# Performance work log

Measured on AMD Instinct MI355X. Metric: run time of the kernel, lower is better.

The kernel has to match this reference:

```python
import jax, jax.numpy as jnp
import numpy as np

NEG_SLOPE = 0.2  # PyG RGATConv default negative_slope


def _rgat_conv(x, src, dst, edge_type, W, q, k, b, num_nodes):
    # W: [R, in, H] per-relation weight (heads=1 so H = heads*out_channels)
    # Transform every node by every relation once, then gather per edge
    # (same math as PyG's per-edge bmm with index_select'd weights, but
    #  avoids materializing [E, in, H] weights).
    xr = jnp.einsum('ni,rio->rno', x, W)            # [R, N, H]
    qv = jnp.einsum('rno,oh->rnh', xr, q)           # [R, N, heads]
    kv = jnp.einsum('rno,oh->rnh', xr, k)           # [R, N, heads]
    # additive self-attention: alpha_e = leaky_relu(q(out_i) + k(out_j))
    alpha = qv[edge_type, dst] + kv[edge_type, src]  # [E, heads]
    alpha = jnp.where(alpha >= 0, alpha, NEG_SLOPE * alpha)
    # softmax over incoming edges of each destination node (across-relation)
    amax = jax.ops.segment_max(alpha, dst, num_segments=num_nodes)  # [N, heads]
    amax = jnp.where(jnp.isfinite(amax), amax, 0.0)
    ex = jnp.exp(alpha - amax[dst])
    denom = jax.ops.segment_sum(ex, dst, num_segments=num_nodes)
    att = ex / (denom[dst] + 1e-16)                 # [E, heads]
    msg = xr[edge_type, src] * att                  # [E, H] (heads=1 broadcast)
    out = jax.ops.segment_sum(msg, dst, num_segments=num_nodes)    # [N, H]
    return out + b


def setup_inputs() -> dict:
    key = jax.random.key(0)
    ks = jax.random.split(key, 16)
    N, E, R, IN, H = 50000, 800000, 8, 128, 128
    x = jax.random.normal(ks[0], (N, IN), dtype=jnp.float32)
    edge_index = jax.random.randint(ks[1], (2, E), 0, N, dtype=jnp.int32)
    edge_type = jax.random.randint(ks[2], (E,), 0, R, dtype=jnp.int32)
    s_in = 1.0 / np.sqrt(IN)
    s_h = 1.0 / np.sqrt(H)
    w0 = jax.random.normal(ks[3], (R, IN, H), dtype=jnp.float32) * s_in
    q0 = jax.random.normal(ks[4], (H, 1), dtype=jnp.float32) * s_h
    k0 = jax.random.normal(ks[5], (H, 1), dtype=jnp.float32) * s_h
    b0 = jnp.zeros((H,), dtype=jnp.float32)
    w1 = jax.random.normal(ks[6], (R, H, H), dtype=jnp.float32) * s_h
    q1 = jax.random.normal(ks[7], (H, 1), dtype=jnp.float32) * s_h
    k1 = jax.random.normal(ks[8], (H, 1), dtype=jnp.float32) * s_h
    b1 = jnp.zeros((H,), dtype=jnp.float32)
    fc1_w = jax.random.normal(ks[9], (2 * H, H), dtype=jnp.float32) * (1.0 / np.sqrt(2 * H))
    fc1_b = jnp.zeros((H,), dtype=jnp.float32)
    fc2_w = jax.random.normal(ks[10], (H, 1), dtype=jnp.float32) * s_h
    fc2_b = jnp.zeros((1,), dtype=jnp.float32)
    return {"x": x, "edge_index": edge_index, "edge_type": edge_type,
            "w0": w0, "q0": q0, "k0": k0, "b0": b0,
            "w1": w1, "q1": q1, "k1": k1, "b1": b1,
            "fc1_w": fc1_w, "fc1_b": fc1_b, "fc2_w": fc2_w, "fc2_b": fc2_b}


def reference(x, edge_index, edge_type, w0, q0, k0, b0, w1, q1, k1, b1, fc1_w, fc1_b, fc2_w, fc2_b):
    N = x.shape[0]
    src, dst = edge_index[0], edge_index[1]
    h = jax.nn.relu(_rgat_conv(x, src, dst, edge_type, w0, q0, k0, b0, N))
    h = jax.nn.relu(_rgat_conv(h, src, dst, edge_type, w1, q1, k1, b1, N))
    g = jnp.concatenate([h.mean(axis=0), h.max(axis=0)], axis=-1)  # [2H]
    g = jnp.tanh(g)
    g = jax.nn.relu(g @ fc1_w + fc1_b)   # dropout is identity in eval mode
    out = g @ fc2_w + fc2_b              # [1]
    return jax.nn.sigmoid(out)
```

## Files before the change

kernel.cpp:

```cpp
#include <hip/hip_runtime.h>
#include <hip/hip_bf16.h>


typedef __bf16 bf16x8 __attribute__((ext_vector_type(8)));
typedef __bf16 bf16x4 __attribute__((ext_vector_type(4)));
typedef __bf16 bf16x2 __attribute__((ext_vector_type(2)));
typedef float f32x4 __attribute__((ext_vector_type(4)));

#define CBSH 10
#define CSC_CH 4096


__global__ __launch_bounds__(256) void k_chist(const int* __restrict__ dst, int* __restrict__ chist, int E) {
  __shared__ int lh[64];
  int t = threadIdx.x;
  if (t < 64) lh[t] = 0;
  __syncthreads();
  for (int e = blockIdx.x * 256 + t; e < E; e += gridDim.x * 256)
    atomicAdd(&lh[dst[e] >> CBSH], 1);
  __syncthreads();
  if (t < 64 && lh[t]) atomicAdd(&chist[t], lh[t]);
}

__global__ void k_cscan(const int* __restrict__ chist, int* __restrict__ cbase, int* __restrict__ ccur,
                        int ncb, int E) {
  if (threadIdx.x == 0) {
    int acc = 0;
    for (int i = 0; i < ncb; ++i) { cbase[i] = acc; ccur[i] = acc; acc += chist[i]; }
    cbase[ncb] = E;
  }
}

__global__ __launch_bounds__(256) void k_cscatter(const int* __restrict__ src, const int* __restrict__ dst,
                                                  const int* __restrict__ et, int* __restrict__ ccur,
                                                  int* __restrict__ tmp, int E) {
  __shared__ int recbuf[CSC_CH];
  __shared__ int lcnt[64], lbase[64], gbase[64], lcur[64];
  int t = threadIdx.x;
  int base = blockIdx.x * CSC_CH;
  int cnt = E - base; if (cnt > CSC_CH) cnt = CSC_CH;
  if (t < 64) lcnt[t] = 0;
  __syncthreads();
  int myrec[CSC_CH / 256], mycb[CSC_CH / 256];
  int k = 0;
  for (int i = t; i < cnt; i += 256, ++k) {
    int d = dst[base + i];
    int cb = d >> CBSH;
    myrec[k] = src[base + i] | (et[base + i] << 17) | ((d & ((1 << CBSH) - 1)) << 20);
    mycb[k] = cb;
    atomicAdd(&lcnt[cb], 1);
  }
  __syncthreads();
  if (t == 0) {
    int acc = 0;
    for (int c = 0; c < 64; ++c) { lbase[c] = acc; lcur[c] = acc; acc += lcnt[c]; }
  }
  __syncthreads();
  if (t < 64 && lcnt[t] > 0) gbase[t] = atomicAdd(&ccur[t], lcnt[t]);
  __syncthreads();
  k = 0;
  for (int i = t; i < cnt; i += 256, ++k) {
    int p = atomicAdd(&lcur[mycb[k]], 1);
    recbuf[p] = myrec[k];
  }
  __syncthreads();
  for (int i = t; i < cnt; i += 256) {
    int lo = 0, hi = 63;
    while (lo < hi) { int mid = (lo + hi + 1) >> 1; if (lbase[mid] <= i) lo = mid; else hi = mid - 1; }
    tmp[gbase[lo] + (i - lbase[lo])] = recbuf[i];
  }
}

__global__ __launch_bounds__(1024) void k_fsort(const int* __restrict__ cbase, const int* __restrict__ tmp,
                                                int* __restrict__ recs, int* __restrict__ row_ptr,
                                                int N, int E) {
  __shared__ int sd[1024];
  __shared__ int ncur[1024];
  int cb = blockIdx.x, t = threadIdx.x;
  int n0 = cb << CBSH;
  int begin = cbase[cb], endd = cbase[cb + 1];
  sd[t] = 0;
  __syncthreads();
  for (int i = begin + t; i < endd; i += 1024)
    atomicAdd(&sd[(tmp[i] >> 20) & 1023], 1);
  __syncthreads();
  int myc = sd[t];
  for (int off = 1; off < 1024; off <<= 1) {
    int xv = 0; if (t >= off) xv = sd[t - off];
    __syncthreads();
    sd[t] += xv;
    __syncthreads();
  }
  int ex = sd[t] - myc;
  int node = n0 + t;
  if (node < N) row_ptr[node] = begin + ex;
  if (node == N - 1) row_ptr[N] = E;
  ncur[t] = begin + ex;
  __syncthreads();
  for (int i = begin + t; i < endd; i += 1024) {
    int rc = tmp[i];
    int p = atomicAdd(&ncur[(rc >> 20) & 1023], 1);
    recs[p] = rc & 0xFFFFF;
  }
}


__global__ __launch_bounds__(256) void k_wprep(const float* __restrict__ W, const float* __restrict__ q,
                                               const float* __restrict__ k, __bf16* __restrict__ wqkb,
                                               __bf16* __restrict__ WT) {
  if (blockIdx.x < 256) {
    int g = blockIdx.x * 4 + (threadIdx.x >> 6);
    int lane = threadIdx.x & 63;
    const float2* wrow = (const float2*)(W + (size_t)g * 128);
    float2 wv = wrow[lane];
    float2 qv2 = ((const float2*)q)[lane];
    float2 kv2 = ((const float2*)k)[lane];
    float aq = wv.x * qv2.x + wv.y * qv2.y;
    float ak = wv.x * kv2.x + wv.y * kv2.y;
    #pragma unroll
    for (int off = 32; off; off >>= 1) {
      aq += __shfl_xor(aq, off, 64);
      ak += __shfl_xor(ak, off, 64);
    }
    if (lane == 0) { wqkb[g] = (__bf16)aq; wqkb[1024 + g] = (__bf16)ak; }
  } else {
    __shared__ float t[32][33];
    int bb = blockIdx.x - 256;
    int r = bb >> 4;
    int rem = bb & 15;
    int k0 = (rem & 3) * 32, h0 = (rem >> 2) * 32;
    int tx = threadIdx.x & 31;
    int ty = threadIdx.x >> 5;
    #pragma unroll
    for (int i = 0; i < 4; ++i) {
      int kk = ty + i * 8;
      t[kk][tx] = W[((size_t)r * 128 + k0 + kk) * 128 + h0 + tx];
    }
    __syncthreads();
    #pragma unroll
    for (int i = 0; i < 4; ++i) {
      int hh = ty + i * 8;
      WT[(size_t)(h0 + hh) * 1024 + r * 128 + k0 + tx] = (__bf16)t[tx][hh];
    }
  }
}

template <int L0>
__global__ __launch_bounds__(256) void k_qkv(const void* __restrict__ xin, const __bf16* __restrict__ wqkb,
                                             float* __restrict__ qkv, __bf16* __restrict__ xbout, int N) {
  int wv = threadIdx.x >> 6, l = threadIdx.x & 63;
  int nb = blockIdx.x * 64 + wv * 16;
  if (nb >= N) return;
  int arow = nb + (l & 15);
  bool valid = arow < N;
  int koff = (l >> 4) * 8;
  const bf16x8* gB = (const bf16x8*)(wqkb + (size_t)(l & 15) * 128 + koff);
  f32x4 acc = (f32x4)0.f;
  #pragma unroll
  for (int kt = 0; kt < 4; ++kt) {
    bf16x8 bv = gB[kt * 4];
    bf16x8 av;
    if (L0) {
      const float* gA = (const float*)xin + (size_t)arow * 128 + koff + kt * 32;
      float4 f0 = make_float4(0.f, 0.f, 0.f, 0.f), f1 = f0;
      if (valid) { f0 = *(const float4*)gA; f1 = *(const float4*)(gA + 4); }
      av[0] = (__bf16)f0.x; av[1] = (__bf16)f0.y; av[2] = (__bf16)f0.z; av[3] = (__bf16)f0.w;
      av[4] = (__bf16)f1.x; av[5] = (__bf16)f1.y; av[6] = (__bf16)f1.z; av[7] = (__bf16)f1.w;
      if (valid) *(bf16x8*)(xbout + (size_t)arow * 128 + koff + kt * 32) = av;
    } else {
      const bf16x8* gA = (const bf16x8*)((const __bf16*)xin + (size_t)arow * 128 + koff);
      av = valid ? gA[kt * 4] : (bf16x8)(__bf16)0.0f;
    }
    acc = __builtin_amdgcn_mfma_f32_16x16x32_bf16(av, bv, acc, 0, 0, 0);
  }
  #pragma unroll
  for (int j = 0; j < 4; ++j) {
    int row = nb + (l >> 4) * 4 + j;
    if (row < N) qkv[(size_t)row * 16 + (l & 15)] = acc[j];
  }
}


#define ASTR 136

__global__ __launch_bounds__(256) void k_gemmY(const __bf16* __restrict__ A,
                                               const __bf16* __restrict__ WT2,
                                               __bf16* __restrict__ Y, int M) {
  __shared__ __bf16 As[128 * ASTR];
  __shared__ __bf16 Bs[128 * ASTR];
  int bm = blockIdx.x * 128;
  int tid = threadIdx.x;
  int w = tid >> 6, l = tid & 63;
  int srow = tid >> 1;
  int cb8 = (tid & 1) * 8;
  bool valid = (bm + srow) < M;

  {
    const bf16x8* gA = (const bf16x8*)(A + (size_t)(bm + srow) * 128);
    #pragma unroll
    for (int i = 0; i < 8; ++i) {
      bf16x8 v = valid ? gA[cb8 + i] : (bf16x8)(__bf16)0.0f;
      *(bf16x8*)&As[srow * ASTR + (cb8 + i) * 8] = v;
    }
  }

  for (int r = 0; r < 8; ++r) {
    __syncthreads();
    {
      const bf16x8* gB = (const bf16x8*)(WT2 + (size_t)srow * 1024 + r * 128);
      #pragma unroll
      for (int i = 0; i < 8; ++i)
        *(bf16x8*)&Bs[srow * ASTR + (cb8 + i) * 8] = gB[cb8 + i];
    }
    __syncthreads();

    f32x4 acc[2][8];
    #pragma unroll
    for (int m2 = 0; m2 < 2; ++m2)
      #pragma unroll
      for (int n2 = 0; n2 < 8; ++n2) acc[m2][n2] = (f32x4)0.f;

    #pragma unroll
    for (int ks = 0; ks < 4; ++ks) {
      bf16x8 af[2], bfv[8];
      #pragma unroll
      for (int m2 = 0; m2 < 2; ++m2)
        af[m2] = *(const bf16x8*)&As[(w * 32 + m2 * 16 + (l & 15)) * ASTR + ks * 32 + (l >> 4) * 8];
      #pragma unroll
      for (int n2 = 0; n2 < 8; ++n2)
        bfv[n2] = *(const bf16x8*)&Bs[(n2 * 16 + (l & 15)) * ASTR + ks * 32 + (l >> 4) * 8];
      #pragma unroll
      for (int m2 = 0; m2 < 2; ++m2)
        #pragma unroll
        for (int n2 = 0; n2 < 8; ++n2)
          acc[m2][n2] = __builtin_amdgcn_mfma_f32_16x16x32_bf16(af[m2], bfv[n2], acc[m2][n2], 0, 0, 0);
    }

    __bf16* Yr = Y + ((size_t)r * M + bm) * 128;
    #pragma unroll
    for (int m2 = 0; m2 < 2; ++m2)
      #pragma unroll
      for (int j = 0; j < 4; ++j) {
        int row = w * 32 + m2 * 16 + (l >> 4) * 4 + j;
        if (bm + row < M) {
          #pragma unroll
          for (int n2 = 0; n2 < 8; ++n2)
            Yr[(size_t)row * 128 + n2 * 16 + (l & 15)] = (__bf16)acc[m2][n2][j];
        }
      }
  }
}


__global__ __launch_bounds__(256) void k_aggY(const int* __restrict__ row_ptr, const int* __restrict__ recs,
                                              const float* __restrict__ qkv, const __bf16* __restrict__ Y,
                                              const float* __restrict__ bias, __bf16* __restrict__ hout,
                                              int N) {
  int wv = threadIdx.x >> 6;
  int lane = threadIdx.x & 63;
  int n = blockIdx.x * 4 + wv;
  if (n >= N) return;
  int start = row_ptr[n], end = row_ptr[n + 1];
  const float* qvn = qkv + (size_t)n * 16;
  float denom = 0.f, m_run = -1e30f;
  int sub = lane & 15;
  int grp = lane >> 4;
  float acc[8];
  #pragma unroll
  for (int j = 0; j < 8; ++j) acc[j] = 0.f;

  for (int c0 = start; c0 < end; c0 += 64) {
    int cend = (end < c0 + 64) ? end : (c0 + 64);
    int cnt = cend - c0;
    int p = c0 + lane;
    float a = -1e30f; int rec = 0;
    if (p < cend) {
      rec = recs[p];
      int s = rec & 0x1FFFF, r = (rec >> 17) & 7;
      float t = qvn[r] + qkv[(size_t)s * 16 + 8 + r];
      a = (t >= 0.f) ? t : 0.2f * t;
    }
    float cm = a;
    #pragma unroll
    for (int off = 32; off; off >>= 1) cm = fmaxf(cm, __shfl_xor(cm, off, 64));
    if (cm > m_run) {
      if (m_run > -1e29f) {
        float scale = __expf(m_run - cm);
        denom *= scale;
        #pragma unroll
        for (int j = 0; j < 8; ++j) acc[j] *= scale;
      }
      m_run = cm;
    }
    float wgt = (p < cend) ? __expf(a - m_run) : 0.f;
    float ws = wgt;
    #pragma unroll
    for (int off = 32; off; off >>= 1) ws += __shfl_xor(ws, off, 64);
    denom += ws;
    int wbits = __float_as_int(wgt);

    int nbatch = (cnt + 3) >> 2;
    int b = 0;
    for (; b + 4 <= nbatch; b += 4) {
      int rg[4], wg[4];
      #pragma unroll
      for (int j = 0; j < 4; ++j) {
        int idx = grp * 4 + (b + j) * 16;
        rg[j] = __builtin_amdgcn_ds_bpermute(idx, rec);
        wg[j] = __builtin_amdgcn_ds_bpermute(idx, wbits);
      }
      bf16x8 xv[4];
      #pragma unroll
      for (int j = 0; j < 4; ++j) {
        int s_ = rg[j] & 0x1FFFF;
        int r_ = (rg[j] >> 17) & 7;
        xv[j] = *(const bf16x8*)(Y + ((size_t)r_ * N + s_) * 128 + sub * 8);
      }
      #pragma unroll
      for (int j = 0; j < 4; ++j) {
        float fw = __int_as_float(wg[j]);
        #pragma unroll
        for (int jj = 0; jj < 8; ++jj) acc[jj] += fw * (float)xv[j][jj];
      }
    }
    for (; b < nbatch; ++b) {
      int idx = grp * 4 + b * 16;
      int rg = __builtin_amdgcn_ds_bpermute(idx, rec);
      int wg = __builtin_amdgcn_ds_bpermute(idx, wbits);
      float fw = __int_as_float(wg);
      int s_ = rg & 0x1FFFF;
      int r_ = (rg >> 17) & 7;
      bf16x8 xv = *(const bf16x8*)(Y + ((size_t)r_ * N + s_) * 128 + sub * 8);
      #pragma unroll
      for (int jj = 0; jj < 8; ++jj) acc[jj] += fw * (float)xv[jj];
    }
  }

  #pragma unroll
  for (int j = 0; j < 8; ++j) {
    acc[j] += __shfl_xor(acc[j], 16, 64);
    acc[j] += __shfl_xor(acc[j], 32, 64);
  }
  float inv = 1.f / (denom + 1e-16f);
  if (grp == 0) {
    float4 b0 = *(const float4*)(bias + sub * 8);
    float4 b1 = *(const float4*)(bias + sub * 8 + 4);
    float bb[8] = {b0.x, b0.y, b0.z, b0.w, b1.x, b1.y, b1.z, b1.w};
    bf16x8 o;
    #pragma unroll
    for (int j = 0; j < 8; ++j) o[j] = (__bf16)fmaxf(acc[j] * inv + bb[j], 0.f);
    *(bf16x8*)(hout + (size_t)n * 128 + sub * 8) = o;
  }
}


__global__ __launch_bounds__(256) void k_pool(const __bf16* __restrict__ h, float* __restrict__ gsum,
                                              float* __restrict__ gmax, int N) {
  int c2 = threadIdx.x & 63;
  int grp = threadIdx.x >> 6;
  float s0 = 0.f, s1 = 0.f, m0 = 0.f, m1 = 0.f;
  for (int n = blockIdx.x * 4 + grp; n < N; n += gridDim.x * 4) {
    bf16x2 v = ((const bf16x2*)(h + (size_t)n * 128))[c2];
    float v0 = (float)v.x, v1 = (float)v.y;
    s0 += v0; s1 += v1;
    m0 = fmaxf(m0, v0); m1 = fmaxf(m1, v1);
  }
  __shared__ float ss0[256], ss1[256], sm0[256], sm1[256];
  ss0[threadIdx.x] = s0; ss1[threadIdx.x] = s1;
  sm0[threadIdx.x] = m0; sm1[threadIdx.x] = m1;
  __syncthreads();
  if (grp == 0) {
    #pragma unroll
    for (int g = 1; g < 4; ++g) {
      s0 += ss0[g * 64 + c2]; s1 += ss1[g * 64 + c2];
      m0 = fmaxf(m0, sm0[g * 64 + c2]); m1 = fmaxf(m1, sm1[g * 64 + c2]);
    }
    atomicAdd(&gsum[2 * c2 + 0], s0);
    atomicAdd(&gsum[2 * c2 + 1], s1);
    atomicMax((int*)gmax + 2 * c2 + 0, __float_as_int(m0));
    atomicMax((int*)gmax + 2 * c2 + 1, __float_as_int(m1));
  }
}

__global__ void k_head(const float* __restrict__ gsum, const float* __restrict__ gmax,
                       const float* __restrict__ fc1w, const float* __restrict__ fc1b,
                       const float* __restrict__ fc2w, const float* __restrict__ fc2b,
                       float* __restrict__ out, int N) {
  __shared__ float g[256];
  __shared__ float red[128];
  int t = threadIdx.x;
  if (t < 128) g[t] = tanhf(gsum[t] / (float)N);
  else g[t] = tanhf(gmax[t - 128]);
  __syncthreads();
  float r1 = 0.f;
  if (t < 128) {
    float a = fc1b[t];
    for (int i = 0; i < 256; i++) a += g[i] * fc1w[i * 128 + t];
    r1 = a > 0.f ? a : 0.f;
    red[t] = r1 * fc2w[t];
  }
  __syncthreads();
  for (int s = 64; s > 0; s >>= 1) {
    if (t < s) red[t] += red[t + s];
    __syncthreads();
  }
  if (t == 0) {
    float o = red[0] + fc2b[0];
    out[0] = 1.f / (1.f + __expf(-o));
  }
}


extern "C" void kernel_launch(void* const* d_in, const int* in_sizes, int n_in,
                              void* d_out, int out_size, void* d_ws, size_t ws_size,
                              hipStream_t stream) {
  const float* x    = (const float*)d_in[0];
  const int*   ei   = (const int*)d_in[1];
  const int*   ety  = (const int*)d_in[2];
  const float* w0   = (const float*)d_in[3];
  const float* q0   = (const float*)d_in[4];
  const float* k0   = (const float*)d_in[5];
  const float* b0   = (const float*)d_in[6];
  const float* w1   = (const float*)d_in[7];
  const float* q1   = (const float*)d_in[8];
  const float* k1   = (const float*)d_in[9];
  const float* b1   = (const float*)d_in[10];
  const float* fc1w = (const float*)d_in[11];
  const float* fc1b = (const float*)d_in[12];
  const float* fc2w = (const float*)d_in[13];
  const float* fc2b = (const float*)d_in[14];
  int N = in_sizes[0] / 128;
  int E = in_sizes[2];
  const int* src = ei;
  const int* dst = ei + E;

  char* base = (char*)d_ws;
  size_t off = 0;
  auto alloc = [&](size_t bytes) -> void* {
    off = (off + 255) & ~(size_t)255;
    void* p = base + off;
    off += bytes;
    return p;
  };
  int ncb = (N + (1 << CBSH) - 1) >> CBSH;

  int*    row_ptr = (int*)alloc((size_t)(N + 1) * 4);
  int*    chist   = (int*)alloc(64 * 4);
  int*    cbase   = (int*)alloc(65 * 4);
  int*    ccur    = (int*)alloc(64 * 4);
  int*    tmp     = (int*)alloc((size_t)E * 4);
  int*    recs    = (int*)alloc((size_t)E * 4);
  float*  qkv     = (float*)alloc((size_t)N * 16 * 4);
  float*  gsum    = (float*)alloc(128 * 4);
  float*  gmax    = (float*)alloc(128 * 4);
  __bf16* wqkb    = (__bf16*)alloc(2048 * 2);
  __bf16* xb      = (__bf16*)alloc((size_t)N * 128 * 2);
  __bf16* h1b     = (__bf16*)alloc((size_t)N * 128 * 2);
  __bf16* h2b     = (__bf16*)alloc((size_t)N * 128 * 2);
  __bf16* WT2     = (__bf16*)alloc((size_t)128 * 1024 * 2);
  __bf16* Y       = (__bf16*)alloc((size_t)8 * N * 128 * 2);

  hipMemsetAsync(chist, 0, 64 * 4, stream);
  k_chist<<<256, 256, 0, stream>>>(dst, chist, E);
  k_cscan<<<1, 64, 0, stream>>>(chist, cbase, ccur, ncb, E);
  k_cscatter<<<(E + CSC_CH - 1) / CSC_CH, 256, 0, stream>>>(src, dst, ety, ccur, tmp, E);
  k_fsort<<<ncb, 1024, 0, stream>>>(cbase, tmp, recs, row_ptr, N, E);

  for (int layer = 0; layer < 2; ++layer) {
    const float*  W    = layer ? w1 : w0;
    const float*  qq   = layer ? q1 : q0;
    const float*  kk   = layer ? k1 : k0;
    const float*  bb   = layer ? b1 : b0;
    const __bf16* xinb = layer ? h1b : xb;
    __bf16*       hout = layer ? h2b : h1b;

    k_wprep<<<384, 256, 0, stream>>>(W, qq, kk, wqkb, WT2);
    if (layer == 0)
      k_qkv<1><<<(N + 63) / 64, 256, 0, stream>>>((const void*)x, wqkb, qkv, xb, N);
    else
      k_qkv<0><<<(N + 63) / 64, 256, 0, stream>>>((const void*)xinb, wqkb, qkv, nullptr, N);
    k_gemmY<<<(N + 127) / 128, 256, 0, stream>>>(xinb, WT2, Y, N);
    k_aggY<<<(N + 3) / 4, 256, 0, stream>>>(row_ptr, recs, qkv, Y, bb, hout, N);
  }

  hipMemsetAsync(gsum, 0, 128 * 4, stream);
  hipMemsetAsync(gmax, 0, 128 * 4, stream);
  k_pool<<<256, 256, 0, stream>>>(h2b, gsum, gmax, N);
  k_head<<<1, 256, 0, stream>>>(gsum, gmax, fc1w, fc1b, fc2w, fc2b, (float*)d_out, N);
}
```

Before: 275.9 us.

## Fuse qkv projection into gemmY, inline chunk scan, merge memsets

Computes the per-node q/k attention projections inside the relation GEMM kernel from the A tile already in shared memory. This removes the separate k_qkv launch, and layer 0 converts fp32 x to bf16 on the fly instead of writing an xb copy. The single-thread chunk-scan kernel is dropped: each scatter and sort block now recomputes the 64-entry prefix from the histogram. Memsets are merged, and the aggregation inner loop is simplified from a manual 4-way batch to an unroll-2 loop, which may reduce memory-level parallelism in the gathers.

```diff
diff --git a/kernel.cpp b/kernel.cpp
--- a/kernel.cpp
+++ b/kernel.cpp
@@ -22,41 +22,35 @@
   if (t < 64 && lh[t]) atomicAdd(&chist[t], lh[t]);
 }
 
-__global__ void k_cscan(const int* __restrict__ chist, int* __restrict__ cbase, int* __restrict__ ccur,
-                        int ncb, int E) {
-  if (threadIdx.x == 0) {
-    int acc = 0;
-    for (int i = 0; i < ncb; ++i) { cbase[i] = acc; ccur[i] = acc; acc += chist[i]; }
-    cbase[ncb] = E;
-  }
-}
-
 __global__ __launch_bounds__(256) void k_cscatter(const int* __restrict__ src, const int* __restrict__ dst,
-                                                  const int* __restrict__ et, int* __restrict__ ccur,
-                                                  int* __restrict__ tmp, int E) {
+                                                  const int* __restrict__ et, const int* __restrict__ chist,
+                                                  int* __restrict__ ccur0, int* __restrict__ tmp, int E) {
   __shared__ int recbuf[CSC_CH];
-  __shared__ int lcnt[64], lbase[64], gbase[64], lcur[64];
+  __shared__ int lcnt[64], lbase[64], gbase[64], lcur[64], cb[64];
   int t = threadIdx.x;
   int base = blockIdx.x * CSC_CH;
   int cnt = E - base; if (cnt > CSC_CH) cnt = CSC_CH;
-  if (t < 64) lcnt[t] = 0;
+  if (t < 64) { lcnt[t] = 0; cb[t] = chist[t]; }
   __syncthreads();
   int myrec[CSC_CH / 256], mycb[CSC_CH / 256];
   int k = 0;
   for (int i = t; i < cnt; i += 256, ++k) {
     int d = dst[base + i];
-    int cb = d >> CBSH;
+    int c = d >> CBSH;
     myrec[k] = src[base + i] | (et[base + i] << 17) | ((d & ((1 << CBSH) - 1)) << 20);
-    mycb[k] = cb;
-    atomicAdd(&lcnt[cb], 1);
+    mycb[k] = c;
+    atomicAdd(&lcnt[c], 1);
   }
   __syncthreads();
   if (t == 0) {
-    int acc = 0;
-    for (int c = 0; c < 64; ++c) { lbase[c] = acc; lcur[c] = acc; acc += lcnt[c]; }
-  }
-  __syncthreads();
-  if (t < 64 && lcnt[t] > 0) gbase[t] = atomicAdd(&ccur[t], lcnt[t]);
+    int acc = 0, acc2 = 0;
+    for (int c = 0; c < 64; ++c) {
+      lbase[c] = acc; lcur[c] = acc; acc += lcnt[c];
+      int h = cb[c]; cb[c] = acc2; acc2 += h;
+    }
+  }
+  __syncthreads();
+  if (t < 64 && lcnt[t] > 0) gbase[t] = cb[t] + atomicAdd(&ccur0[t], lcnt[t]);
   __syncthreads();
   k = 0;
   for (int i = t; i < cnt; i += 256, ++k) {
@@ -71,16 +65,24 @@
   }
 }
 
-__global__ __launch_bounds__(1024) void k_fsort(const int* __restrict__ cbase, const int* __restrict__ tmp,
+__global__ __launch_bounds__(1024) void k_fsort(const int* __restrict__ chist, const int* __restrict__ tmp,
                                                 int* __restrict__ recs, int* __restrict__ row_ptr,
                                                 int N, int E) {
   __shared__ int sd[1024];
   __shared__ int ncur[1024];
+  __shared__ int cbs[65];
   int cb = blockIdx.x, t = threadIdx.x;
   int n0 = cb << CBSH;
-  int begin = cbase[cb], endd = cbase[cb + 1];
+  if (t < 64) cbs[t] = chist[t];
+  __syncthreads();
+  if (t == 0) {
+    int acc = 0;
+    for (int c = 0; c < 64; ++c) { int h = cbs[c]; cbs[c] = acc; acc += h; }
+    cbs[64] = acc;
+  }
   sd[t] = 0;
   __syncthreads();
+  int begin = cbs[cb], endd = cbs[cb + 1];
   for (int i = begin + t; i < endd; i += 1024)
     atomicAdd(&sd[(tmp[i] >> 20) & 1023], 1);
   __syncthreads();
@@ -145,47 +147,14 @@
   }
 }
 
+
+#define ASTR 136
+
 template <int L0>
-__global__ __launch_bounds__(256) void k_qkv(const void* __restrict__ xin, const __bf16* __restrict__ wqkb,
-                                             float* __restrict__ qkv, __bf16* __restrict__ xbout, int N) {
-  int wv = threadIdx.x >> 6, l = threadIdx.x & 63;
-  int nb = blockIdx.x * 64 + wv * 16;
-  if (nb >= N) return;
-  int arow = nb + (l & 15);
-  bool valid = arow < N;
-  int koff = (l >> 4) * 8;
-  const bf16x8* gB = (const bf16x8*)(wqkb + (size_t)(l & 15) * 128 + koff);
-  f32x4 acc = (f32x4)0.f;
-  #pragma unroll
-  for (int kt = 0; kt < 4; ++kt) {
-    bf16x8 bv = gB[kt * 4];
-    bf16x8 av;
-    if (L0) {
-      const float* gA = (const float*)xin + (size_t)arow * 128 + koff + kt * 32;
-      float4 f0 = make_float4(0.f, 0.f, 0.f, 0.f), f1 = f0;
-      if (valid) { f0 = *(const float4*)gA; f1 = *(const float4*)(gA + 4); }
-      av[0] = (__bf16)f0.x; av[1] = (__bf16)f0.y; av[2] = (__bf16)f0.z; av[3] = (__bf16)f0.w;
-      av[4] = (__bf16)f1.x; av[5] = (__bf16)f1.y; av[6] = (__bf16)f1.z; av[7] = (__bf16)f1.w;
-      if (valid) *(bf16x8*)(xbout + (size_t)arow * 128 + koff + kt * 32) = av;
-    } else {
-      const bf16x8* gA = (const bf16x8*)((const __bf16*)xin + (size_t)arow * 128 + koff);
-      av = valid ? gA[kt * 4] : (bf16x8)(__bf16)0.0f;
-    }
-    acc = __builtin_amdgcn_mfma_f32_16x16x32_bf16(av, bv, acc, 0, 0, 0);
-  }
-  #pragma unroll
-  for (int j = 0; j < 4; ++j) {
-    int row = nb + (l >> 4) * 4 + j;
-    if (row < N) qkv[(size_t)row * 16 + (l & 15)] = acc[j];
-  }
-}
-
-
-#define ASTR 136
-
-__global__ __launch_bounds__(256) void k_gemmY(const __bf16* __restrict__ A,
+__global__ __launch_bounds__(256) void k_gemmY(const void* __restrict__ xin,
                                                const __bf16* __restrict__ WT2,
-                                               __bf16* __restrict__ Y, int M) {
+                                               const __bf16* __restrict__ wqkb,
+                                               __bf16* __restrict__ Y, float* __restrict__ qkv, int M) {
   __shared__ __bf16 As[128 * ASTR];
   __shared__ __bf16 Bs[128 * ASTR];
   int bm = blockIdx.x * 128;
@@ -195,13 +164,50 @@
   int cb8 = (tid & 1) * 8;
   bool valid = (bm + srow) < M;
 
-  {
-    const bf16x8* gA = (const bf16x8*)(A + (size_t)(bm + srow) * 128);
+  if (L0) {
+    const float* gA = (const float*)xin + (size_t)(bm + srow) * 128 + cb8 * 8;
+    #pragma unroll
+    for (int i = 0; i < 8; ++i) {
+      float4 f0 = make_float4(0.f, 0.f, 0.f, 0.f), f1 = f0;
+      if (valid) { f0 = *(const float4*)(gA + i * 8); f1 = *(const float4*)(gA + i * 8 + 4); }
+      bf16x8 v;
+      v[0] = (__bf16)f0.x; v[1] = (__bf16)f0.y; v[2] = (__bf16)f0.z; v[3] = (__bf16)f0.w;
+      v[4] = (__bf16)f1.x; v[5] = (__bf16)f1.y; v[6] = (__bf16)f1.z; v[7] = (__bf16)f1.w;
+      *(bf16x8*)&As[srow * ASTR + (cb8 + i) * 8] = v;
+    }
+  } else {
+    const bf16x8* gA = (const bf16x8*)((const __bf16*)xin + (size_t)(bm + srow) * 128);
     #pragma unroll
     for (int i = 0; i < 8; ++i) {
       bf16x8 v = valid ? gA[cb8 + i] : (bf16x8)(__bf16)0.0f;
       *(bf16x8*)&As[srow * ASTR + (cb8 + i) * 8] = v;
     }
+  }
+  {
+    int qr = tid >> 4, qc = tid & 15;
+    *(bf16x8*)&Bs[qr * ASTR + qc * 8] = *(const bf16x8*)(wqkb + (size_t)qr * 128 + qc * 8);
+  }
+  __syncthreads();
+
+  {
+    f32x4 qacc[2];
+    qacc[0] = (f32x4)0.f; qacc[1] = (f32x4)0.f;
+    #pragma unroll
+    for (int ks = 0; ks < 4; ++ks) {
+      bf16x8 bq = *(const bf16x8*)&Bs[(l & 15) * ASTR + ks * 32 + (l >> 4) * 8];
+      #pragma unroll
+      for (int m2 = 0; m2 < 2; ++m2) {
+        bf16x8 af = *(const bf16x8*)&As[(w * 32 + m2 * 16 + (l & 15)) * ASTR + ks * 32 + (l >> 4) * 8];
+        qacc[m2] = __builtin_amdgcn_mfma_f32_16x16x32_bf16(af, bq, qacc[m2], 0, 0, 0);
+      }
+    }
+    #pragma unroll
+    for (int m2 = 0; m2 < 2; ++m2)
+      #pragma unroll
+      for (int j = 0; j < 4; ++j) {
+        int row = w * 32 + m2 * 16 + (l >> 4) * 4 + j;
+        if (bm + row < M) qkv[(size_t)(bm + row) * 16 + (l & 15)] = qacc[m2][j];
+      }
   }
 
   for (int r = 0; r < 8; ++r) {
@@ -300,30 +306,8 @@
     int wbits = __float_as_int(wgt);
 
     int nbatch = (cnt + 3) >> 2;
-    int b = 0;
-    for (; b + 4 <= nbatch; b += 4) {
-      int rg[4], wg[4];
-      #pragma unroll
-      for (int j = 0; j < 4; ++j) {
-        int idx = grp * 4 + (b + j) * 16;
-        rg[j] = __builtin_amdgcn_ds_bpermute(idx, rec);
-        wg[j] = __builtin_amdgcn_ds_bpermute(idx, wbits);
-      }
-      bf16x8 xv[4];
-      #pragma unroll
-      for (int j = 0; j < 4; ++j) {
-        int s_ = rg[j] & 0x1FFFF;
-        int r_ = (rg[j] >> 17) & 7;
-        xv[j] = *(const bf16x8*)(Y + ((size_t)r_ * N + s_) * 128 + sub * 8);
-      }
-      #pragma unroll
-      for (int j = 0; j < 4; ++j) {
-        float fw = __int_as_float(wg[j]);
-        #pragma unroll
-        for (int jj = 0; jj < 8; ++jj) acc[jj] += fw * (float)xv[j][jj];
-      }
-    }
-    for (; b < nbatch; ++b) {
+    #pragma unroll 2
+    for (int b = 0; b < nbatch; ++b) {
       int idx = grp * 4 + b * 16;
       int rg = __builtin_amdgcn_ds_bpermute(idx, rec);
       int wg = __builtin_amdgcn_ds_bpermute(idx, wbits);
@@ -332,7 +316,7 @@
       int r_ = (rg >> 17) & 7;
       bf16x8 xv = *(const bf16x8*)(Y + ((size_t)r_ * N + s_) * 128 + sub * 8);
       #pragma unroll
-      for (int jj = 0; jj < 8; ++jj) acc[jj] += fw * (float)xv[jj];
+      for (int j = 0; j < 8; ++j) acc[j] += fw * (float)xv[j];
     }
   }
 
@@ -445,46 +429,42 @@
   int ncb = (N + (1 << CBSH) - 1) >> CBSH;
 
   int*    row_ptr = (int*)alloc((size_t)(N + 1) * 4);
-  int*    chist   = (int*)alloc(64 * 4);
-  int*    cbase   = (int*)alloc(65 * 4);
-  int*    ccur    = (int*)alloc(64 * 4);
+  int*    csrctr  = (int*)alloc(128 * 4);
+  int*    chist   = csrctr;
+  int*    ccur0   = csrctr + 64;
   int*    tmp     = (int*)alloc((size_t)E * 4);
   int*    recs    = (int*)alloc((size_t)E * 4);
   float*  qkv     = (float*)alloc((size_t)N * 16 * 4);
-  float*  gsum    = (float*)alloc(128 * 4);
-  float*  gmax    = (float*)alloc(128 * 4);
+  float*  gpool   = (float*)alloc(256 * 4);
+  float*  gsum    = gpool;
+  float*  gmax    = gpool + 128;
   __bf16* wqkb    = (__bf16*)alloc(2048 * 2);
-  __bf16* xb      = (__bf16*)alloc((size_t)N * 128 * 2);
   __bf16* h1b     = (__bf16*)alloc((size_t)N * 128 * 2);
   __bf16* h2b     = (__bf16*)alloc((size_t)N * 128 * 2);
   __bf16* WT2     = (__bf16*)alloc((size_t)128 * 1024 * 2);
   __bf16* Y       = (__bf16*)alloc((size_t)8 * N * 128 * 2);
 
-  hipMemsetAsync(chist, 0, 64 * 4, stream);
+  hipMemsetAsync(csrctr, 0, 128 * 4, stream);
   k_chist<<<256, 256, 0, stream>>>(dst, chist, E);
-  k_cscan<<<1, 64, 0, stream>>>(chist, cbase, ccur, ncb, E);
-  k_cscatter<<<(E + CSC_CH - 1) / CSC_CH, 256, 0, stream>>>(src, dst, ety, ccur, tmp, E);
-  k_fsort<<<ncb, 1024, 0, stream>>>(cbase, tmp, recs, row_ptr, N, E);
+  k_cscatter<<<(E + CSC_CH - 1) / CSC_CH, 256, 0, stream>>>(src, dst, ety, chist, ccur0, tmp, E);
+  k_fsort<<<ncb, 1024, 0, stream>>>(chist, tmp, recs, row_ptr, N, E);
 
   for (int layer = 0; layer < 2; ++layer) {
     const float*  W    = layer ? w1 : w0;
     const float*  qq   = layer ? q1 : q0;
     const float*  kk   = layer ? k1 : k0;
     const float*  bb   = layer ? b1 : b0;
-    const __bf16* xinb = layer ? h1b : xb;
     __bf16*       hout = layer ? h2b : h1b;
 
     k_wprep<<<384, 256, 0, stream>>>(W, qq, kk, wqkb, WT2);
     if (layer == 0)
-      k_qkv<1><<<(N + 63) / 64, 256, 0, stream>>>((const void*)x, wqkb, qkv, xb, N);
+      k_gemmY<1><<<(N + 127) / 128, 256, 0, stream>>>((const void*)x, WT2, wqkb, Y, qkv, N);
     else
-      k_qkv<0><<<(N + 63) / 64, 256, 0, stream>>>((const void*)xinb, wqkb, qkv, nullptr, N);
-    k_gemmY<<<(N + 127) / 128, 256, 0, stream>>>(xinb, WT2, Y, N);
+      k_gemmY<0><<<(N + 127) / 128, 256, 0, stream>>>((const void*)h1b, WT2, wqkb, Y, qkv, N);
     k_aggY<<<(N + 3) / 4, 256, 0, stream>>>(row_ptr, recs, qkv, Y, bb, hout, N);
   }
 
-  hipMemsetAsync(gsum, 0, 128 * 4, stream);
-  hipMemsetAsync(gmax, 0, 128 * 4, stream);
+  hipMemsetAsync(gpool, 0, 256 * 4, stream);
   k_pool<<<256, 256, 0, stream>>>(h2b, gsum, gmax, N);
   k_head<<<1, 256, 0, stream>>>(gsum, gmax, fc1w, fc1b, fc2w, fc2b, (float*)d_out, N);
 }
```

Result: faster. 258.6 us (-6.3%).
